# Kernel optimization log

Hardware: AMD Instinct MI355X
Metric: run time of the kernel (lower is better)

Reference implementation:

```python
import jax, jax.numpy as jnp
import numpy as np

N = 50000
E = 800000
D = 128
EPS = 1e-12  # torch F.normalize eps


def setup_inputs() -> dict:
    key = jax.random.key(0)
    ks = jax.random.split(key, 8)
    x = jax.random.normal(ks[0], (N, D), dtype=jnp.float32)
    edge_index = jax.random.randint(ks[1], (2, E), 0, N, dtype=jnp.int64)
    s = 1.0 / np.sqrt(D)
    # project MLP (Linear(D, D) + bias, followed by relu in SAGEConv)
    Wp = jax.random.uniform(ks[2], (D, D), jnp.float32, -s, s)
    bp = jax.random.uniform(ks[3], (D,), jnp.float32, -s, s)
    # lin_l: applied to aggregated neighbor features (with bias)
    Wl = jax.random.uniform(ks[4], (D, D), jnp.float32, -s, s)
    bl = jax.random.uniform(ks[5], (D,), jnp.float32, -s, s)
    # lin_r: applied to root features (no bias)
    Wr = jax.random.uniform(ks[6], (D, D), jnp.float32, -s, s)
    return {"x": x, "edge_index": edge_index, "Wp": Wp, "bp": bp,
            "Wl": Wl, "bl": bl, "Wr": Wr}


def reference(x, edge_index, Wp, bp, Wl, bl, Wr):
    src, dst = edge_index[0], edge_index[1]
    n = x.shape[0]
    # project=True: per-node projection + relu (applied before gather, same math)
    h = jax.nn.relu(x @ Wp.T + bp)                      # [N, D]
    # gather messages from source nodes, mean-aggregate at targets
    msg = h[src]                                        # [E, D]
    agg = jax.ops.segment_sum(msg, dst, num_segments=n)  # [N, D]
    cnt = jax.ops.segment_sum(jnp.ones((msg.shape[0],), x.dtype), dst,
                              num_segments=n)
    mean = agg / jnp.maximum(cnt, 1.0)[:, None]         # nodes w/o edges -> 0
    # combine: lin_l(agg) + lin_r(x)
    out = mean @ Wl.T + bl + x @ Wr.T                   # [N, D]
    # elementwise tail: ELU -> (dropout p=0, eval) -> L2 normalize -> residual
    out = jax.nn.elu(out)
    norm = jnp.sqrt(jnp.sum(out * out, axis=-1, keepdims=True))
    out = out / jnp.maximum(norm, EPS)
    return x + out
```

## Files before the change

### kernel.cpp

```cpp
#include <hip/hip_runtime.h>
#include <hip/hip_bf16.h>

#define DD 128
#define EPSN 1e-12f
#define MAXDEG 64
#define EPB 2048

typedef __attribute__((ext_vector_type(8))) short bf16x8;
typedef __attribute__((ext_vector_type(4))) float f32x4;

__device__ __forceinline__ short bfbits(float f) {
  unsigned u = __float_as_uint(f);
  u += 0x7FFF + ((u >> 16) & 1);
  return (short)(u >> 16);
}
__device__ __forceinline__ float bf2f(short s) {
  return __uint_as_float(((unsigned)(unsigned short)s) << 16);
}

__global__ __launch_bounds__(256) void k_init(
    const float* __restrict__ Wp, const float* __restrict__ Wl,
    const float* __restrict__ Wr, short* __restrict__ Wb, int m,
    int* __restrict__ cnt, int* __restrict__ cnt8, int n)
{
  int i = blockIdx.x * 256 + threadIdx.x;
  if (i < m) {
    Wb[i]         = bfbits(Wp[i]);
    Wb[m + i]     = bfbits(Wl[i]);
    Wb[2 * m + i] = bfbits(Wr[i]);
  }
  if (i < n) cnt[i] = 0;
  if (i < 8) cnt8[i] = 0;
}

__global__ __launch_bounds__(256) void k_projA(
    const float* __restrict__ x, const short* __restrict__ Wpb,
    const float* __restrict__ bp, unsigned short* __restrict__ h,
    const int* __restrict__ ei, unsigned* __restrict__ seg,
    int* __restrict__ cnt8, int n, int nE, int nABlk,
    unsigned scale, int segCap)
{
  int b = blockIdx.x;
  int tid = threadIdx.x;

  if (b < nABlk) {
    __shared__ int bcnt[8];
    __shared__ int bcur[8];
    if (tid < 8) bcnt[tid] = 0;
    __syncthreads();
    int base = b * EPB;
    int dv[8], sv[8], bv[8];
    bool val[8];
#pragma unroll
    for (int u = 0; u < 8; ++u) {
      int e = base + u * 256 + tid;
      val[u] = (e < nE);
      if (val[u]) {
        dv[u] = ei[nE + e];
        sv[u] = ei[e];
        bv[u] = (int)(((unsigned long long)(unsigned)dv[u] * scale) >> 32);
        atomicAdd(&bcnt[bv[u]], 1);
      }
    }
    __syncthreads();
    if (tid < 8) bcur[tid] = atomicAdd(&cnt8[tid], bcnt[tid]);
    __syncthreads();
#pragma unroll
    for (int u = 0; u < 8; ++u) {
      if (val[u]) {
        int pos = atomicAdd(&bcur[bv[u]], 1);
        if (pos < segCap)
          seg[(size_t)bv[u] * segCap + pos] =
              ((unsigned)dv[u] << 16) | (unsigned)sv[u];
      }
    }
    return;
  }

  int l = tid & 63;
  int wid = ((b - nABlk) * 256 + tid) >> 6;
  int row0 = wid * 16;
  if (row0 >= n) return;
  int lr = l & 15, kg = l >> 4;
  int rA = row0 + lr; if (rA > n - 1) rA = n - 1;

  f32x4 acc[8];
#pragma unroll
  for (int cb = 0; cb < 8; ++cb) {
    float bv2 = bp[16 * cb + lr];
    acc[cb] = (f32x4){bv2, bv2, bv2, bv2};
  }

  const float* xrow = x + (size_t)rA * DD;
#pragma unroll
  for (int ks = 0; ks < 4; ++ks) {
    int ko = 32 * ks + 8 * kg;
    float4 f0 = *(const float4*)(xrow + ko);
    float4 f1 = *(const float4*)(xrow + ko + 4);
    float fv[8] = {f0.x, f0.y, f0.z, f0.w, f1.x, f1.y, f1.z, f1.w};
    bf16x8 ah, al;
#pragma unroll
    for (int j = 0; j < 8; ++j) {
      short hb = bfbits(fv[j]);
      ah[j] = hb;
      al[j] = bfbits(fv[j] - bf2f(hb));
    }
#pragma unroll
    for (int cb = 0; cb < 8; ++cb) {
      bf16x8 bfr = *(const bf16x8*)(Wpb + ((16 * cb + lr) * DD + ko));
      acc[cb] = __builtin_amdgcn_mfma_f32_16x16x32_bf16(ah, bfr, acc[cb], 0, 0, 0);
      acc[cb] = __builtin_amdgcn_mfma_f32_16x16x32_bf16(al, bfr, acc[cb], 0, 0, 0);
    }
  }

#pragma unroll
  for (int i = 0; i < 4; ++i) {
    int r = row0 + 4 * kg + i;
    if (r < n) {
#pragma unroll
      for (int cb = 0; cb < 8; ++cb) {
        float v = fmaxf(acc[cb][i], 0.f);
        h[(size_t)r * DD + 16 * cb + lr] = (unsigned short)bfbits(v);
      }
    }
  }
}

__global__ __launch_bounds__(256) void k_passB(
    const unsigned* __restrict__ seg, const int* __restrict__ cnt8,
    int* __restrict__ cnt, unsigned short* __restrict__ slots, int segCap)
{
  int b = blockIdx.x;
  int tid = threadIdx.x;
  int r = b & 7;
  int chunk = b >> 3;
  int len = cnt8[r]; if (len > segCap) len = segCap;
  const unsigned* s = seg + (size_t)r * segCap;
  int base = chunk * EPB;
#pragma unroll
  for (int u = 0; u < 8; ++u) {
    int e = base + u * 256 + tid;
    if (e < len) {
      unsigned p = s[e];
      int d = (int)(p >> 16);
      int src = (int)(p & 0xFFFFu);
      int pos = atomicAdd(&cnt[d], 1);
      if (pos < MAXDEG) slots[(size_t)d * MAXDEG + pos] = (unsigned short)src;
    }
  }
}

__global__ __launch_bounds__(256) void k_gather(
    const int* __restrict__ cnt, const unsigned short* __restrict__ slots,
    const __hip_bfloat162* __restrict__ h2,
    __hip_bfloat162* __restrict__ meanb, int n)
{
  int w = (blockIdx.x * 256 + threadIdx.x) >> 6;
  int l = threadIdx.x & 63;
  int node0 = w * 4;
  if (node0 >= n) return;

#pragma unroll 1
  for (int i = 0; i < 4; ++i) {
    int node = node0 + i;
    if (node >= n) break;
    int dgTrue = cnt[node];
    int dg = dgTrue < MAXDEG ? dgTrue : MAXDEG;
    int myidx = (int)slots[(size_t)node * MAXDEG + l];

    float s0 = 0.f, s1 = 0.f, t0 = 0.f, t1 = 0.f;
    int j = 0;
    for (; j + 8 <= dg; j += 8) {
      int i0 = __builtin_amdgcn_readlane(myidx, j);
      int i1 = __builtin_amdgcn_readlane(myidx, j + 1);
      int i2 = __builtin_amdgcn_readlane(myidx, j + 2);
      int i3 = __builtin_amdgcn_readlane(myidx, j + 3);
      int i4 = __builtin_amdgcn_readlane(myidx, j + 4);
      int i5 = __builtin_amdgcn_readlane(myidx, j + 5);
      int i6 = __builtin_amdgcn_readlane(myidx, j + 6);
      int i7 = __builtin_amdgcn_readlane(myidx, j + 7);
      __hip_bfloat162 v0 = h2[(size_t)i0 * 64 + l];
      __hip_bfloat162 v1 = h2[(size_t)i1 * 64 + l];
      __hip_bfloat162 v2 = h2[(size_t)i2 * 64 + l];
      __hip_bfloat162 v3 = h2[(size_t)i3 * 64 + l];
      __hip_bfloat162 v4 = h2[(size_t)i4 * 64 + l];
      __hip_bfloat162 v5 = h2[(size_t)i5 * 64 + l];
      __hip_bfloat162 v6 = h2[(size_t)i6 * 64 + l];
      __hip_bfloat162 v7 = h2[(size_t)i7 * 64 + l];
      s0 += __bfloat162float(v0.x) + __bfloat162float(v1.x);
      s1 += __bfloat162float(v0.y) + __bfloat162float(v1.y);
      t0 += __bfloat162float(v2.x) + __bfloat162float(v3.x);
      t1 += __bfloat162float(v2.y) + __bfloat162float(v3.y);
      s0 += __bfloat162float(v4.x) + __bfloat162float(v5.x);
      s1 += __bfloat162float(v4.y) + __bfloat162float(v5.y);
      t0 += __bfloat162float(v6.x) + __bfloat162float(v7.x);
      t1 += __bfloat162float(v6.y) + __bfloat162float(v7.y);
    }
    for (; j < dg; ++j) {
      int i0 = __builtin_amdgcn_readlane(myidx, j);
      __hip_bfloat162 v0 = h2[(size_t)i0 * 64 + l];
      s0 += __bfloat162float(v0.x);
      s1 += __bfloat162float(v0.y);
    }
    s0 += t0; s1 += t1;
    float rd = 1.0f / fmaxf((float)dgTrue, 1.0f);
    __hip_bfloat162 o;
    o.x = __float2bfloat16(s0 * rd);
    o.y = __float2bfloat16(s1 * rd);
    meanb[(size_t)node * 64 + l] = o;
  }
}

__global__ __launch_bounds__(512) void k_combine(
    const float* __restrict__ x, const short* __restrict__ Wlb,
    const float* __restrict__ bl, const short* __restrict__ Wrb,
    const unsigned short* __restrict__ meanb,
    float* __restrict__ out, int n)
{
  __shared__ uint4 Wu[4096];
  __shared__ float ssh[4 * 32];

  int tid = threadIdx.x;

  const uint4* gl = (const uint4*)Wlb;
  const uint4* gr = (const uint4*)Wrb;
#pragma unroll
  for (int it = 0; it < 8; ++it) {
    int g = it * 512 + tid;
    int mat = g >> 11;
    int rem = g & 2047;
    int row = rem >> 4, j = rem & 15;
    uint4 v = mat ? gr[rem] : gl[rem];
    Wu[(mat << 11) | (row << 4) | (j ^ (row & 15))] = v;
  }
  __syncthreads();

  int l = tid & 63;
  int wv = tid >> 6;
  int rg = wv >> 1;
  int half = wv & 1;
  int row0 = (blockIdx.x * 4 + rg) * 16;
  int lr = l & 15, kg = l >> 4;
  bool active = (row0 < n);

  f32x4 acc[4];
  float ss[4] = {0.f, 0.f, 0.f, 0.f};

  if (active) {
    int rA = row0 + lr; if (rA > n - 1) rA = n - 1;
#pragma unroll
    for (int q = 0; q < 4; ++q) {
      float bv = bl[16 * (4 * half + q) + lr];
      acc[q] = (f32x4){bv, bv, bv, bv};
    }

    const unsigned short* mrow = meanb + (size_t)rA * DD;
    const float* xrow = x + (size_t)rA * DD;
#pragma unroll
    for (int ks = 0; ks < 4; ++ks) {
      int ko = 32 * ks + 8 * kg;
      bf16x8 a = *(const bf16x8*)(mrow + ko);
      float4 f0 = *(const float4*)(xrow + ko);
      float4 f1 = *(const float4*)(xrow + ko + 4);
      float fv[8] = {f0.x, f0.y, f0.z, f0.w, f1.x, f1.y, f1.z, f1.w};
      bf16x8 ah, al;
#pragma unroll
      for (int jj = 0; jj < 8; ++jj) {
        short hb = bfbits(fv[jj]);
        ah[jj] = hb;
        al[jj] = bfbits(fv[jj] - bf2f(hb));
      }
      int ju = 4 * ks + kg;
#pragma unroll
      for (int q = 0; q < 4; ++q) {
        int row = 16 * (4 * half + q) + lr;
        bf16x8 bL = *(const bf16x8*)&Wu[(0 << 11) | (row << 4) | (ju ^ lr)];
        bf16x8 bR = *(const bf16x8*)&Wu[(1 << 11) | (row << 4) | (ju ^ lr)];
        acc[q] = __builtin_amdgcn_mfma_f32_16x16x32_bf16(a,  bL, acc[q], 0, 0, 0);
        acc[q] = __builtin_amdgcn_mfma_f32_16x16x32_bf16(ah, bR, acc[q], 0, 0, 0);
        acc[q] = __builtin_amdgcn_mfma_f32_16x16x32_bf16(al, bR, acc[q], 0, 0, 0);
      }
    }

#pragma unroll
    for (int q = 0; q < 4; ++q) {
#pragma unroll
      for (int i = 0; i < 4; ++i) {
        float z = acc[q][i];
        z = z > 0.f ? z : expm1f(z);
        acc[q][i] = z;
        ss[i] += z * z;
      }
    }
#pragma unroll
    for (int i = 0; i < 4; ++i) {
#pragma unroll
      for (int m2 = 1; m2 < 16; m2 <<= 1) ss[i] += __shfl_xor(ss[i], m2);
    }
    if (lr == 0) {
#pragma unroll
      for (int i = 0; i < 4; ++i) ssh[rg * 32 + half * 16 + 4 * kg + i] = ss[i];
    }
  }
  __syncthreads();

  if (active) {
#pragma unroll
    for (int i = 0; i < 4; ++i) {
      int r = row0 + 4 * kg + i;
      if (r < n) {
        float tot = ssh[rg * 32 + 4 * kg + i] + ssh[rg * 32 + 16 + 4 * kg + i];
        float inv = 1.f / fmaxf(sqrtf(tot), EPSN);
#pragma unroll
        for (int q = 0; q < 4; ++q) {
          int c = 16 * (4 * half + q) + lr;
          out[(size_t)r * DD + c] = x[(size_t)r * DD + c] + acc[q][i] * inv;
        }
      }
    }
  }
}

extern "C" void kernel_launch(void* const* d_in, const int* in_sizes, int n_in,
                              void* d_out, int out_size, void* d_ws, size_t ws_size,
                              hipStream_t stream) {
  const float* x  = (const float*)d_in[0];
  const int*   ei = (const int*)d_in[1];
  const float* Wp = (const float*)d_in[2];
  const float* bp = (const float*)d_in[3];
  const float* Wl = (const float*)d_in[4];
  const float* bl = (const float*)d_in[5];
  const float* Wr = (const float*)d_in[6];
  float* out = (float*)d_out;

  int n  = in_sizes[0] / DD;
  int nE = in_sizes[1] / 2;
  int m  = DD * DD;
  int segCap = nE / 8 + 16384;
  unsigned scale = (unsigned)((((unsigned long long)8) << 32) / (unsigned long long)n);

  auto align256 = [](size_t v) { return (v + 255) & ~(size_t)255; };
  char* p = (char*)d_ws;
  unsigned short* h = (unsigned short*)p;      p += align256((size_t)n * DD * 2);
  unsigned short* meanb = (unsigned short*)p;  p += align256((size_t)n * DD * 2);
  int* cnt  = (int*)p;                         p += align256((size_t)n * 4);
  int* cnt8 = (int*)p;                         p += 256;
  unsigned short* slots = (unsigned short*)p;  p += align256((size_t)n * MAXDEG * 2);
  unsigned* seg = (unsigned*)p;                p += align256((size_t)8 * segCap * 4);
  short* Wb = (short*)p;                       p += align256((size_t)3 * m * 2);
  short* Wpb = Wb, *Wlb = Wb + m, *Wrb = Wb + 2 * m;

  k_init<<<256, 256, 0, stream>>>(Wp, Wl, Wr, Wb, m, cnt, cnt8, n);

  int nWaves   = (n + 15) / 16;
  int nProjBlk = (nWaves + 3) / 4;
  int nABlk    = (nE + EPB - 1) / EPB;
  k_projA<<<nABlk + nProjBlk, 256, 0, stream>>>(
      x, Wpb, bp, h, ei, seg, cnt8, n, nE, nABlk, scale, segCap);

  int nChunkB = (segCap + EPB - 1) / EPB;
  k_passB<<<8 * nChunkB, 256, 0, stream>>>(seg, cnt8, cnt, slots, segCap);

  int nGWaves = (n + 3) / 4;
  int nGBlk   = (nGWaves + 3) / 4;
  k_gather<<<nGBlk, 256, 0, stream>>>(
      cnt, slots, (const __hip_bfloat162*)h, (__hip_bfloat162*)meanb, n);

  int nCombBlk = (nWaves + 3) / 4;
  k_combine<<<nCombBlk, 512, 0, stream>>>(x, Wlb, bl, Wrb, meanb, out, n);
}
```

Baseline: 130.2 us.

## Fuse gather into combine kernel and drop weight-conversion init kernel

The neighbor-mean gather moves into the combine kernel, which stages each block's bf16 mean rows in swizzled LDS instead of writing and rereading a global meanb buffer. Weight bf16 conversion moves into the projection and combine kernels, which convert straight from fp32 into LDS. The count zeroing folds into the partition blocks, with a memset for the bucket counters. This removes one kernel launch plus the meanb global round trip, at the cost of redundant per-block weight conversion, more LDS use and 512-thread blocks.

```diff
diff --git a/kernel.cpp b/kernel.cpp
--- a/kernel.cpp
+++ b/kernel.cpp
@@ -4,7 +4,8 @@
 #define DD 128
 #define EPSN 1e-12f
 #define MAXDEG 64
-#define EPB 2048
+#define EPB_A 4096
+#define EPB_B 2048
 
 typedef __attribute__((ext_vector_type(8))) short bf16x8;
 typedef __attribute__((ext_vector_type(4))) float f32x4;
@@ -17,43 +18,35 @@
 __device__ __forceinline__ float bf2f(short s) {
   return __uint_as_float(((unsigned)(unsigned short)s) << 16);
 }
-
-__global__ __launch_bounds__(256) void k_init(
-    const float* __restrict__ Wp, const float* __restrict__ Wl,
-    const float* __restrict__ Wr, short* __restrict__ Wb, int m,
-    int* __restrict__ cnt, int* __restrict__ cnt8, int n)
-{
-  int i = blockIdx.x * 256 + threadIdx.x;
-  if (i < m) {
-    Wb[i]         = bfbits(Wp[i]);
-    Wb[m + i]     = bfbits(Wl[i]);
-    Wb[2 * m + i] = bfbits(Wr[i]);
-  }
-  if (i < n) cnt[i] = 0;
-  if (i < 8) cnt8[i] = 0;
-}
-
-__global__ __launch_bounds__(256) void k_projA(
-    const float* __restrict__ x, const short* __restrict__ Wpb,
+__device__ __forceinline__ unsigned packbf(float a, float b) {
+  return (unsigned)(unsigned short)bfbits(a) |
+         ((unsigned)(unsigned short)bfbits(b) << 16);
+}
+
+__global__ __launch_bounds__(512) void k_projA(
+    const float* __restrict__ x, const float* __restrict__ Wp,
     const float* __restrict__ bp, unsigned short* __restrict__ h,
     const int* __restrict__ ei, unsigned* __restrict__ seg,
-    int* __restrict__ cnt8, int n, int nE, int nABlk,
-    unsigned scale, int segCap)
+    int* __restrict__ cnt8, int* __restrict__ cnt,
+    int n, int nE, int nABlk, unsigned scale, int segCap)
 {
+  __shared__ uint4 WuP[2048];
   int b = blockIdx.x;
   int tid = threadIdx.x;
 
   if (b < nABlk) {
-    __shared__ int bcnt[8];
-    __shared__ int bcur[8];
+    int* bcnt = (int*)&WuP[0];
+    int* bcur = bcnt + 8;
     if (tid < 8) bcnt[tid] = 0;
+    int zi = b * 256 + tid;
+    if (tid < 256 && zi < n) cnt[zi] = 0;
     __syncthreads();
-    int base = b * EPB;
+    int base = b * EPB_A;
     int dv[8], sv[8], bv[8];
     bool val[8];
 #pragma unroll
     for (int u = 0; u < 8; ++u) {
-      int e = base + u * 256 + tid;
+      int e = base + u * 512 + tid;
       val[u] = (e < nE);
       if (val[u]) {
         dv[u] = ei[nE + e];
@@ -77,9 +70,23 @@
     return;
   }
 
+#pragma unroll
+  for (int it = 0; it < 4; ++it) {
+    int g = it * 512 + tid;
+    int row = g >> 4, j = g & 15;
+    const float* src = Wp + row * DD + j * 8;
+    float4 f0 = *(const float4*)src;
+    float4 f1 = *(const float4*)(src + 4);
+    uint4 v;
+    v.x = packbf(f0.x, f0.y); v.y = packbf(f0.z, f0.w);
+    v.z = packbf(f1.x, f1.y); v.w = packbf(f1.z, f1.w);
+    WuP[(row << 4) | (j ^ (row & 15))] = v;
+  }
+  __syncthreads();
+
   int l = tid & 63;
-  int wid = ((b - nABlk) * 256 + tid) >> 6;
-  int row0 = wid * 16;
+  int wv = tid >> 6;
+  int row0 = ((b - nABlk) * 8 + wv) * 16;
   if (row0 >= n) return;
   int lr = l & 15, kg = l >> 4;
   int rA = row0 + lr; if (rA > n - 1) rA = n - 1;
@@ -105,9 +112,11 @@
       ah[j] = hb;
       al[j] = bfbits(fv[j] - bf2f(hb));
     }
+    int ju = 4 * ks + kg;
 #pragma unroll
     for (int cb = 0; cb < 8; ++cb) {
-      bf16x8 bfr = *(const bf16x8*)(Wpb + ((16 * cb + lr) * DD + ko));
+      int row = 16 * cb + lr;
+      bf16x8 bfr = *(const bf16x8*)&WuP[(row << 4) | (ju ^ lr)];
       acc[cb] = __builtin_amdgcn_mfma_f32_16x16x32_bf16(ah, bfr, acc[cb], 0, 0, 0);
       acc[cb] = __builtin_amdgcn_mfma_f32_16x16x32_bf16(al, bfr, acc[cb], 0, 0, 0);
     }
@@ -136,7 +145,7 @@
   int chunk = b >> 3;
   int len = cnt8[r]; if (len > segCap) len = segCap;
   const unsigned* s = seg + (size_t)r * segCap;
-  int base = chunk * EPB;
+  int base = chunk * EPB_B;
 #pragma unroll
   for (int u = 0; u < 8; ++u) {
     int e = base + u * 256 + tid;
@@ -150,90 +159,30 @@
   }
 }
 
-__global__ __launch_bounds__(256) void k_gather(
+__global__ __launch_bounds__(512) void k_gcomb(
+    const float* __restrict__ x, const float* __restrict__ Wl,
+    const float* __restrict__ bl, const float* __restrict__ Wr,
     const int* __restrict__ cnt, const unsigned short* __restrict__ slots,
     const __hip_bfloat162* __restrict__ h2,
-    __hip_bfloat162* __restrict__ meanb, int n)
-{
-  int w = (blockIdx.x * 256 + threadIdx.x) >> 6;
-  int l = threadIdx.x & 63;
-  int node0 = w * 4;
-  if (node0 >= n) return;
-
-#pragma unroll 1
-  for (int i = 0; i < 4; ++i) {
-    int node = node0 + i;
-    if (node >= n) break;
-    int dgTrue = cnt[node];
-    int dg = dgTrue < MAXDEG ? dgTrue : MAXDEG;
-    int myidx = (int)slots[(size_t)node * MAXDEG + l];
-
-    float s0 = 0.f, s1 = 0.f, t0 = 0.f, t1 = 0.f;
-    int j = 0;
-    for (; j + 8 <= dg; j += 8) {
-      int i0 = __builtin_amdgcn_readlane(myidx, j);
-      int i1 = __builtin_amdgcn_readlane(myidx, j + 1);
-      int i2 = __builtin_amdgcn_readlane(myidx, j + 2);
-      int i3 = __builtin_amdgcn_readlane(myidx, j + 3);
-      int i4 = __builtin_amdgcn_readlane(myidx, j + 4);
-      int i5 = __builtin_amdgcn_readlane(myidx, j + 5);
-      int i6 = __builtin_amdgcn_readlane(myidx, j + 6);
-      int i7 = __builtin_amdgcn_readlane(myidx, j + 7);
-      __hip_bfloat162 v0 = h2[(size_t)i0 * 64 + l];
-      __hip_bfloat162 v1 = h2[(size_t)i1 * 64 + l];
-      __hip_bfloat162 v2 = h2[(size_t)i2 * 64 + l];
-      __hip_bfloat162 v3 = h2[(size_t)i3 * 64 + l];
-      __hip_bfloat162 v4 = h2[(size_t)i4 * 64 + l];
-      __hip_bfloat162 v5 = h2[(size_t)i5 * 64 + l];
-      __hip_bfloat162 v6 = h2[(size_t)i6 * 64 + l];
-      __hip_bfloat162 v7 = h2[(size_t)i7 * 64 + l];
-      s0 += __bfloat162float(v0.x) + __bfloat162float(v1.x);
-      s1 += __bfloat162float(v0.y) + __bfloat162float(v1.y);
-      t0 += __bfloat162float(v2.x) + __bfloat162float(v3.x);
-      t1 += __bfloat162float(v2.y) + __bfloat162float(v3.y);
-      s0 += __bfloat162float(v4.x) + __bfloat162float(v5.x);
-      s1 += __bfloat162float(v4.y) + __bfloat162float(v5.y);
-      t0 += __bfloat162float(v6.x) + __bfloat162float(v7.x);
-      t1 += __bfloat162float(v6.y) + __bfloat162float(v7.y);
-    }
-    for (; j < dg; ++j) {
-      int i0 = __builtin_amdgcn_readlane(myidx, j);
-      __hip_bfloat162 v0 = h2[(size_t)i0 * 64 + l];
-      s0 += __bfloat162float(v0.x);
-      s1 += __bfloat162float(v0.y);
-    }
-    s0 += t0; s1 += t1;
-    float rd = 1.0f / fmaxf((float)dgTrue, 1.0f);
-    __hip_bfloat162 o;
-    o.x = __float2bfloat16(s0 * rd);
-    o.y = __float2bfloat16(s1 * rd);
-    meanb[(size_t)node * 64 + l] = o;
-  }
-}
-
-__global__ __launch_bounds__(512) void k_combine(
-    const float* __restrict__ x, const short* __restrict__ Wlb,
-    const float* __restrict__ bl, const short* __restrict__ Wrb,
-    const unsigned short* __restrict__ meanb,
     float* __restrict__ out, int n)
 {
   __shared__ uint4 Wu[4096];
-  __shared__ float ssh[4 * 32];
-
+  __shared__ unsigned mw[4096];
   int tid = threadIdx.x;
 
-  const uint4* gl = (const uint4*)Wlb;
-  const uint4* gr = (const uint4*)Wrb;
 #pragma unroll
   for (int it = 0; it < 8; ++it) {
     int g = it * 512 + tid;
-    int mat = g >> 11;
-    int rem = g & 2047;
+    int mat = g >> 11, rem = g & 2047;
     int row = rem >> 4, j = rem & 15;
-    uint4 v = mat ? gr[rem] : gl[rem];
+    const float* src = (mat ? Wr : Wl) + row * DD + j * 8;
+    float4 f0 = *(const float4*)src;
+    float4 f1 = *(const float4*)(src + 4);
+    uint4 v;
+    v.x = packbf(f0.x, f0.y); v.y = packbf(f0.z, f0.w);
+    v.z = packbf(f1.x, f1.y); v.w = packbf(f1.z, f1.w);
     Wu[(mat << 11) | (row << 4) | (j ^ (row & 15))] = v;
   }
-  __syncthreads();
 
   int l = tid & 63;
   int wv = tid >> 6;
@@ -243,6 +192,57 @@
   int lr = l & 15, kg = l >> 4;
   bool active = (row0 < n);
 
+#pragma unroll 1
+  for (int i = 0; i < 8; ++i) {
+    int r = half * 8 + i;
+    int node = row0 + r;
+    unsigned word = 0;
+    if (node < n) {
+      int dgTrue = cnt[node];
+      int dg = dgTrue < MAXDEG ? dgTrue : MAXDEG;
+      int myidx = (int)slots[(size_t)node * MAXDEG + l];
+      float s0 = 0.f, s1 = 0.f, t0 = 0.f, t1 = 0.f;
+      int j = 0;
+      for (; j + 8 <= dg; j += 8) {
+        int i0 = __builtin_amdgcn_readlane(myidx, j);
+        int i1 = __builtin_amdgcn_readlane(myidx, j + 1);
+        int i2 = __builtin_amdgcn_readlane(myidx, j + 2);
+        int i3 = __builtin_amdgcn_readlane(myidx, j + 3);
+        int i4 = __builtin_amdgcn_readlane(myidx, j + 4);
+        int i5 = __builtin_amdgcn_readlane(myidx, j + 5);
+        int i6 = __builtin_amdgcn_readlane(myidx, j + 6);
+        int i7 = __builtin_amdgcn_readlane(myidx, j + 7);
+        __hip_bfloat162 v0 = h2[(size_t)i0 * 64 + l];
+        __hip_bfloat162 v1 = h2[(size_t)i1 * 64 + l];
+        __hip_bfloat162 v2 = h2[(size_t)i2 * 64 + l];
+        __hip_bfloat162 v3 = h2[(size_t)i3 * 64 + l];
+        __hip_bfloat162 v4 = h2[(size_t)i4 * 64 + l];
+        __hip_bfloat162 v5 = h2[(size_t)i5 * 64 + l];
+        __hip_bfloat162 v6 = h2[(size_t)i6 * 64 + l];
+        __hip_bfloat162 v7 = h2[(size_t)i7 * 64 + l];
+        s0 += __bfloat162float(v0.x) + __bfloat162float(v1.x);
+        s1 += __bfloat162float(v0.y) + __bfloat162float(v1.y);
+        t0 += __bfloat162float(v2.x) + __bfloat162float(v3.x);
+        t1 += __bfloat162float(v2.y) + __bfloat162float(v3.y);
+        s0 += __bfloat162float(v4.x) + __bfloat162float(v5.x);
+        s1 += __bfloat162float(v4.y) + __bfloat162float(v5.y);
+        t0 += __bfloat162float(v6.x) + __bfloat162float(v7.x);
+        t1 += __bfloat162float(v6.y) + __bfloat162float(v7.y);
+      }
+      for (; j < dg; ++j) {
+        int i0 = __builtin_amdgcn_readlane(myidx, j);
+        __hip_bfloat162 v0 = h2[(size_t)i0 * 64 + l];
+        s0 += __bfloat162float(v0.x);
+        s1 += __bfloat162float(v0.y);
+      }
+      s0 += t0; s1 += t1;
+      float rd = 1.0f / fmaxf((float)dgTrue, 1.0f);
+      word = packbf(s0 * rd, s1 * rd);
+    }
+    mw[rg * 1024 + r * 64 + (((l >> 2) ^ (r & 15)) << 2) + (l & 3)] = word;
+  }
+  __syncthreads();
+
   f32x4 acc[4];
   float ss[4] = {0.f, 0.f, 0.f, 0.f};
 
@@ -254,12 +254,13 @@
       acc[q] = (f32x4){bv, bv, bv, bv};
     }
 
-    const unsigned short* mrow = meanb + (size_t)rA * DD;
+    const uint4* mw4 = (const uint4*)mw;
     const float* xrow = x + (size_t)rA * DD;
 #pragma unroll
     for (int ks = 0; ks < 4; ++ks) {
       int ko = 32 * ks + 8 * kg;
-      bf16x8 a = *(const bf16x8*)(mrow + ko);
+      int ju = 4 * ks + kg;
+      bf16x8 a = *(const bf16x8*)&mw4[rg * 256 + lr * 16 + (ju ^ lr)];
       float4 f0 = *(const float4*)(xrow + ko);
       float4 f1 = *(const float4*)(xrow + ko + 4);
       float fv[8] = {f0.x, f0.y, f0.z, f0.w, f1.x, f1.y, f1.z, f1.w};
@@ -270,7 +271,6 @@
         ah[jj] = hb;
         al[jj] = bfbits(fv[jj] - bf2f(hb));
       }
-      int ju = 4 * ks + kg;
 #pragma unroll
       for (int q = 0; q < 4; ++q) {
         int row = 16 * (4 * half + q) + lr;
@@ -297,10 +297,13 @@
 #pragma unroll
       for (int m2 = 1; m2 < 16; m2 <<= 1) ss[i] += __shfl_xor(ss[i], m2);
     }
-    if (lr == 0) {
-#pragma unroll
-      for (int i = 0; i < 4; ++i) ssh[rg * 32 + half * 16 + 4 * kg + i] = ss[i];
-    }
+  }
+  __syncthreads();
+
+  float* ssh = (float*)mw;
+  if (active && lr == 0) {
+#pragma unroll
+    for (int i = 0; i < 4; ++i) ssh[rg * 32 + half * 16 + 4 * kg + i] = ss[i];
   }
   __syncthreads();
 
@@ -335,37 +338,28 @@
 
   int n  = in_sizes[0] / DD;
   int nE = in_sizes[1] / 2;
-  int m  = DD * DD;
   int segCap = nE / 8 + 16384;
   unsigned scale = (unsigned)((((unsigned long long)8) << 32) / (unsigned long long)n);
 
   auto align256 = [](size_t v) { return (v + 255) & ~(size_t)255; };
   char* p = (char*)d_ws;
   unsigned short* h = (unsigned short*)p;      p += align256((size_t)n * DD * 2);
-  unsigned short* meanb = (unsigned short*)p;  p += align256((size_t)n * DD * 2);
   int* cnt  = (int*)p;                         p += align256((size_t)n * 4);
   int* cnt8 = (int*)p;                         p += 256;
   unsigned short* slots = (unsigned short*)p;  p += align256((size_t)n * MAXDEG * 2);
   unsigned* seg = (unsigned*)p;                p += align256((size_t)8 * segCap * 4);
-  short* Wb = (short*)p;                       p += align256((size_t)3 * m * 2);
-  short* Wpb = Wb, *Wlb = Wb + m, *Wrb = Wb + 2 * m;
-
-  k_init<<<256, 256, 0, stream>>>(Wp, Wl, Wr, Wb, m, cnt, cnt8, n);
-
-  int nWaves   = (n + 15) / 16;
-  int nProjBlk = (nWaves + 3) / 4;
-  int nABlk    = (nE + EPB - 1) / EPB;
-  k_projA<<<nABlk + nProjBlk, 256, 0, stream>>>(
-      x, Wpb, bp, h, ei, seg, cnt8, n, nE, nABlk, scale, segCap);
-
-  int nChunkB = (segCap + EPB - 1) / EPB;
+
+  hipMemsetAsync(cnt8, 0, 256, stream);
+
+  int nABlk = (nE + EPB_A - 1) / EPB_A;
+  int nPBlk = (n + 127) / 128;
+  k_projA<<<nABlk + nPBlk, 512, 0, stream>>>(
+      x, Wp, bp, h, ei, seg, cnt8, cnt, n, nE, nABlk, scale, segCap);
+
+  int nChunkB = (segCap + EPB_B - 1) / EPB_B;
   k_passB<<<8 * nChunkB, 256, 0, stream>>>(seg, cnt8, cnt, slots, segCap);
 
-  int nGWaves = (n + 3) / 4;
-  int nGBlk   = (nGWaves + 3) / 4;
-  k_gather<<<nGBlk, 256, 0, stream>>>(
-      cnt, slots, (const __hip_bfloat162*)h, (__hip_bfloat162*)meanb, n);
-
-  int nCombBlk = (nWaves + 3) / 4;
-  k_combine<<<nCombBlk, 512, 0, stream>>>(x, Wlb, bl, Wrb, meanb, out, n);
-}
+  int nCBlk = (n + 63) / 64;
+  k_gcomb<<<nCBlk, 512, 0, stream>>>(
+      x, Wl, bl, Wr, cnt, slots, (const __hip_bfloat162*)h, out, n);
+}
```

Result: faster. 122.3 us (-6.0%).
